# Kernel tuning notes

Measured on AMD Instinct MI355X. Metric: run time of the kernel, lower is better.

## Reference

```python
import jax, jax.numpy as jnp
import numpy as np

N, B, F = 204800, 4096, 256

def setup_inputs() -> dict:
    key = jax.random.key(0)
    ks = jax.random.split(key, 8)
    s = 1.0 / np.sqrt(F)
    return {
        'node_feats': jax.random.normal(ks[0], (N, F), jnp.float32),
        'g_feats': jax.random.normal(ks[1], (B, F), jnp.float32),
        'segment_ids': jnp.sort(jax.random.randint(ks[2], (N,), 0, B, jnp.int32)),
        'W_logit': jax.random.normal(ks[3], (1, 2 * F), jnp.float32) * (1.0 / np.sqrt(2 * F)),
        'b_logit': jnp.zeros((1,), jnp.float32),
        'W_proj': jax.random.normal(ks[4], (F, F), jnp.float32) * s,
        'b_proj': jnp.zeros((F,), jnp.float32),
        'W_ih': jax.random.normal(ks[5], (3 * F, F), jnp.float32) * s,
        'W_hh': jax.random.normal(ks[6], (3 * F, F), jnp.float32) * s,
        'b_ih': jnp.zeros((3 * F,), jnp.float32),
        'b_hh': jnp.zeros((3 * F,), jnp.float32),
    }

def reference(node_feats, g_feats, segment_ids, W_logit, b_logit, W_proj, b_proj, W_ih, W_hh, b_ih, b_hh):
    num_graphs = g_feats.shape[0]
    # logits: Linear(2F -> 1) on [broadcast(relu(g_feats)), node_feats], then LeakyReLU(0.01)
    ctx_nodes = jax.nn.relu(g_feats)[segment_ids]                      # [N, F]
    z = jnp.concatenate([ctx_nodes, node_feats], axis=1) @ W_logit.T + b_logit  # [N, 1]
    z = jax.nn.leaky_relu(z, negative_slope=0.01)
    # per-graph segment softmax over nodes
    zmax = jax.ops.segment_max(z, segment_ids, num_segments=num_graphs)
    z_exp = jnp.exp(z - zmax[segment_ids])
    denom = jax.ops.segment_sum(z_exp, segment_ids, num_segments=num_graphs)
    a = z_exp / denom[segment_ids]                                     # [N, 1]
    # project nodes (Dropout is identity at eval) and weighted segment sum
    hv = node_feats @ W_proj.T + b_proj                                # [N, F]
    g_repr = jax.ops.segment_sum(a * hv, segment_ids, num_segments=num_graphs)  # [B, F]
    context = jax.nn.elu(g_repr)
    # PyTorch GRUCell: input=context, hidden=g_feats
    gi = context @ W_ih.T + b_ih                                       # [B, 3F]
    gh = g_feats @ W_hh.T + b_hh
    i_r, i_z, i_n = jnp.split(gi, 3, axis=1)
    h_r, h_z, h_n = jnp.split(gh, 3, axis=1)
    r = jax.nn.sigmoid(i_r + h_r)
    zg = jax.nn.sigmoid(i_z + h_z)
    n = jnp.tanh(i_n + r * h_n)
    return (1.0 - zg) * n + zg * g_feats
```

## Files before the change

### kernel.cpp

```cpp
#include <hip/hip_runtime.h>

#define NN 204800
#define BB 4096
#define FF 256
#define CAP 72

typedef unsigned short u16;
typedef unsigned int u32;
typedef short bf16x8 __attribute__((ext_vector_type(8)));
typedef float f32x4  __attribute__((ext_vector_type(4)));

__device__ __forceinline__ u16 rne_bf16(float f){
    union { u32 v; float f; } t; t.f = f;
    u32 lsb = (t.v >> 16) & 1u;
    t.v += 0x7fffu + lsb;
    return (u16)(t.v >> 16);
}
__device__ __forceinline__ float bf16_to_f(u16 h){
    union { u32 v; float f; } t; t.v = (u32)h << 16; return t.f;
}
__device__ __forceinline__ void cvt4(const float* __restrict__ src, u16* __restrict__ dst){
    float4 v = *(const float4*)src;
    ushort4 h;
    h.x = rne_bf16(v.x); h.y = rne_bf16(v.y);
    h.z = rne_bf16(v.z); h.w = rne_bf16(v.w);
    *(ushort4*)dst = h;
}

__global__ void k_prep(const float* __restrict__ gfe, const float* __restrict__ Wp,
                       const float* __restrict__ Wih, const float* __restrict__ Whh,
                       const int* __restrict__ seg, int* __restrict__ start,
                       u16* __restrict__ gfe_b, u16* __restrict__ Wp_b,
                       u16* __restrict__ Wih_b, u16* __restrict__ Whh_b){
    int i = blockIdx.x * 256 + threadIdx.x;
    if (i <= BB){
        int lo = 0, hi = NN;
        while (lo < hi){ int mid = (lo + hi) >> 1; if (seg[mid] < i) lo = mid + 1; else hi = mid; }
        start[i] = lo;
    }
    const int n_gfe = BB * FF;
    const int n_wp  = FF * FF;
    const int n_w3  = 3 * FF * FF;
    int j = i * 4;
    if (j < n_gfe){ cvt4(gfe + j, gfe_b + j); return; }
    j -= n_gfe;
    if (j < n_wp){ cvt4(Wp + j, Wp_b + j); return; }
    j -= n_wp;
    if (j < n_w3){ cvt4(Wih + j, Wih_b + j); return; }
    j -= n_w3;
    if (j < n_w3){ cvt4(Whh + j, Whh_b + j); return; }
}
#define PREP_V4 ((BB*FF + FF*FF + 2*3*FF*FF) / 4)

__global__ __launch_bounds__(256) void k_attn(
        const float* __restrict__ x, const float* __restrict__ Wl,
        const float* __restrict__ bl, const float* __restrict__ gfe,
        const int* __restrict__ start, u16* __restrict__ s_b){
    __shared__ __align__(16) u16 xs[CAP][FF];
    __shared__ float zs[512];
    __shared__ float red[16];
    int g = blockIdx.x;
    int s0 = start[g], cnt = start[g + 1] - s0;
    int tid = threadIdx.x, wave = tid >> 6, lane = tid & 63;
    if (cnt == 0){
        s_b[(size_t)g * FF + tid] = 0;
        return;
    }
    float p = Wl[tid] * fmaxf(gfe[(size_t)g * FF + tid], 0.f);
    #pragma unroll
    for (int o = 32; o; o >>= 1) p += __shfl_xor(p, o);
    if (lane == 0) red[8 + wave] = p;
    float blv = bl[0];
    float4 wv = *(const float4*)(Wl + FF + lane * 4);

    auto st_row = [&](int row, const float4& v){
        ushort4 h;
        h.x = rne_bf16(v.x); h.y = rne_bf16(v.y);
        h.z = rne_bf16(v.z); h.w = rne_bf16(v.w);
        *(ushort4*)(&xs[row][lane * 4]) = h;
    };

    int i = wave;
    for (; i + 12 < cnt; i += 16){
        const float* r0 = x + (size_t)(s0 + i) * FF + lane * 4;
        float4 xv0 = *(const float4*)(r0);
        float4 xv1 = *(const float4*)(r0 + 4 * FF);
        float4 xv2 = *(const float4*)(r0 + 8 * FF);
        float4 xv3 = *(const float4*)(r0 + 12 * FF);
        float d0 = xv0.x * wv.x + xv0.y * wv.y + xv0.z * wv.z + xv0.w * wv.w;
        float d1 = xv1.x * wv.x + xv1.y * wv.y + xv1.z * wv.z + xv1.w * wv.w;
        float d2 = xv2.x * wv.x + xv2.y * wv.y + xv2.z * wv.z + xv2.w * wv.w;
        float d3 = xv3.x * wv.x + xv3.y * wv.y + xv3.z * wv.z + xv3.w * wv.w;
        #pragma unroll
        for (int o = 32; o; o >>= 1){
            d0 += __shfl_xor(d0, o); d1 += __shfl_xor(d1, o);
            d2 += __shfl_xor(d2, o); d3 += __shfl_xor(d3, o);
        }
        if (i      < CAP) st_row(i,      xv0);
        if (i + 4  < CAP) st_row(i + 4,  xv1);
        if (i + 8  < CAP) st_row(i + 8,  xv2);
        if (i + 12 < CAP) st_row(i + 12, xv3);
        if (lane == 0){
            zs[i] = d0; zs[i + 4] = d1; zs[i + 8] = d2; zs[i + 12] = d3;
        }
    }
    for (; i < cnt; i += 4){
        float4 xv = *(const float4*)(x + (size_t)(s0 + i) * FF + lane * 4);
        float d = xv.x * wv.x + xv.y * wv.y + xv.z * wv.z + xv.w * wv.w;
        #pragma unroll
        for (int o = 32; o; o >>= 1) d += __shfl_xor(d, o);
        if (i < CAP) st_row(i, xv);
        if (lane == 0) zs[i] = d;
    }
    __syncthreads();
    float cg = red[8] + red[9] + red[10] + red[11] + blv;
    float mx = -3.4e38f;
    for (int k = tid; k < cnt; k += 256){
        float t = cg + zs[k];
        t = t >= 0.f ? t : 0.01f * t;
        zs[k] = t;
        mx = fmaxf(mx, t);
    }
    #pragma unroll
    for (int o = 32; o; o >>= 1) mx = fmaxf(mx, __shfl_xor(mx, o));
    if (lane == 0) red[wave] = mx;
    __syncthreads();
    mx = fmaxf(fmaxf(red[0], red[1]), fmaxf(red[2], red[3]));
    float dsum = 0.f;
    for (int k = tid; k < cnt; k += 256){
        float e = expf(zs[k] - mx);
        zs[k] = e;
        dsum += e;
    }
    #pragma unroll
    for (int o = 32; o; o >>= 1) dsum += __shfl_xor(dsum, o);
    if (lane == 0) red[4 + wave] = dsum;
    __syncthreads();
    float inv = 1.f / (red[4] + red[5] + red[6] + red[7]);
    float acc = 0.f;
    int lim = cnt < CAP ? cnt : CAP;
    for (int k = 0; k < lim; k++) acc += zs[k] * bf16_to_f(xs[k][tid]);
    for (int k = CAP; k < cnt; k++) acc += zs[k] * x[(size_t)(s0 + k) * FF + tid];
    s_b[(size_t)g * FF + tid] = rne_bf16(acc * inv);
}

__global__ __launch_bounds__(256) void k_proj_mfma(
        const u16* __restrict__ s_b, const u16* __restrict__ Wp_b,
        const float* __restrict__ bp, const int* __restrict__ gate,
        u16* __restrict__ ctx_b){
    int tid = threadIdx.x;
    int w = tid >> 6, l = tid & 63;
    int mn = l & 15, q = l >> 4;
    int m0 = blockIdx.x * 64 + w * 16;
    int f0 = blockIdx.y * 64;
    f32x4 acc[4] = {};
    const u16* arow = s_b + (size_t)(m0 + mn) * FF + q * 8;
    #pragma unroll
    for (int kb = 0; kb < 8; kb++){
        bf16x8 a = *(const bf16x8*)(arow + kb * 32);
        #pragma unroll
        for (int cc = 0; cc < 4; cc++){
            bf16x8 b = *(const bf16x8*)(Wp_b + (size_t)(f0 + cc * 16 + mn) * FF + kb * 32 + q * 8);
            acc[cc] = __builtin_amdgcn_mfma_f32_16x16x32_bf16(a, b, acc[cc], 0, 0, 0);
        }
    }
    #pragma unroll
    for (int cc = 0; cc < 4; cc++){
        int f = f0 + cc * 16 + mn;
        float bias = bp[f];
        #pragma unroll
        for (int r = 0; r < 4; r++){
            int g = m0 + q * 4 + r;
            float bs = (gate[g + 1] > gate[g]) ? 1.f : 0.f;
            float v = acc[cc][r] + bs * bias;
            v = v > 0.f ? v : expm1f(v);
            ctx_b[(size_t)g * FF + f] = rne_bf16(v);
        }
    }
}

__global__ __launch_bounds__(256) void k_gru_mfma(
        const u16* __restrict__ ctx_b, const u16* __restrict__ gfe_b,
        const u16* __restrict__ Wih_b, const u16* __restrict__ Whh_b,
        const float* __restrict__ bih, const float* __restrict__ bhh,
        const float* __restrict__ gfe, float* __restrict__ out){
    int tid = threadIdx.x;
    int w = tid >> 6, l = tid & 63;
    int mn = l & 15, q = l >> 4;
    int g0 = blockIdx.x * 64 + w * 16;
    int f0 = blockIdx.y * 64;
    f32x4 ai[3][4] = {};
    f32x4 ah[3][4] = {};
    const u16* ac_row = ctx_b + (size_t)(g0 + mn) * FF + q * 8;
    const u16* ag_row = gfe_b + (size_t)(g0 + mn) * FF + q * 8;
    #pragma unroll
    for (int kb = 0; kb < 8; kb++){
        bf16x8 a_c = *(const bf16x8*)(ac_row + kb * 32);
        bf16x8 a_g = *(const bf16x8*)(ag_row + kb * 32);
        #pragma unroll
        for (int s = 0; s < 3; s++){
            #pragma unroll
            for (int cc = 0; cc < 4; cc++){
                size_t woff = (size_t)(s * FF + f0 + cc * 16 + mn) * FF + kb * 32 + q * 8;
                bf16x8 bi = *(const bf16x8*)(Wih_b + woff);
                ai[s][cc] = __builtin_amdgcn_mfma_f32_16x16x32_bf16(a_c, bi, ai[s][cc], 0, 0, 0);
                bf16x8 bh = *(const bf16x8*)(Whh_b + woff);
                ah[s][cc] = __builtin_amdgcn_mfma_f32_16x16x32_bf16(a_g, bh, ah[s][cc], 0, 0, 0);
            }
        }
    }
    #pragma unroll
    for (int cc = 0; cc < 4; cc++){
        int f = f0 + cc * 16 + mn;
        float bir = bih[f], biz = bih[FF + f], bin_ = bih[2 * FF + f];
        float bhr = bhh[f], bhz = bhh[FF + f], bhn = bhh[2 * FF + f];
        #pragma unroll
        for (int r = 0; r < 4; r++){
            int g = g0 + q * 4 + r;
            float rg = 1.f / (1.f + expf(-(ai[0][cc][r] + bir + ah[0][cc][r] + bhr)));
            float zg = 1.f / (1.f + expf(-(ai[1][cc][r] + biz + ah[1][cc][r] + bhz)));
            float ng = tanhf(ai[2][cc][r] + bin_ + rg * (ah[2][cc][r] + bhn));
            float h = gfe[(size_t)g * FF + f];
            out[(size_t)g * FF + f] = (1.f - zg) * ng + zg * h;
        }
    }
}

extern "C" void kernel_launch(void* const* d_in, const int* in_sizes, int n_in,
                              void* d_out, int out_size, void* d_ws, size_t ws_size,
                              hipStream_t stream){
    const float* node = (const float*)d_in[0];
    const float* gfe  = (const float*)d_in[1];
    const int*   seg  = (const int*)d_in[2];
    const float* Wl   = (const float*)d_in[3];
    const float* bl   = (const float*)d_in[4];
    const float* Wp   = (const float*)d_in[5];
    const float* bp   = (const float*)d_in[6];
    const float* Wih  = (const float*)d_in[7];
    const float* Whh  = (const float*)d_in[8];
    const float* bih  = (const float*)d_in[9];
    const float* bhh  = (const float*)d_in[10];
    float* out = (float*)d_out;

    char* p = (char*)d_ws;
    auto alloc = [&](size_t bytes)->void*{
        void* r = (void*)p; p += (bytes + 255) & ~(size_t)255; return r;
    };
    int*   start = (int*)  alloc((BB + 1) * sizeof(int));
    u16*   s_b   = (u16*)  alloc((size_t)BB * FF * sizeof(u16));
    u16*   ctx_b = (u16*)  alloc((size_t)BB * FF * sizeof(u16));
    u16*   gfe_b = (u16*)  alloc((size_t)BB * FF * sizeof(u16));
    u16*   Wp_b  = (u16*)  alloc((size_t)FF * FF * sizeof(u16));
    u16*   Wih_b = (u16*)  alloc((size_t)3 * FF * FF * sizeof(u16));
    u16*   Whh_b = (u16*)  alloc((size_t)3 * FF * FF * sizeof(u16));

    k_prep<<<(PREP_V4 + 255) / 256, 256, 0, stream>>>(gfe, Wp, Wih, Whh, seg, start,
                                                      gfe_b, Wp_b, Wih_b, Whh_b);
    k_attn<<<BB, 256, 0, stream>>>(node, Wl, bl, gfe, start, s_b);
    k_proj_mfma<<<dim3(BB / 64, FF / 64), 256, 0, stream>>>(s_b, Wp_b, bp, start, ctx_b);
    k_gru_mfma<<<dim3(BB / 64, FF / 64), 256, 0, stream>>>(ctx_b, gfe_b, Wih_b, Whh_b,
                                                           bih, bhh, gfe, out);
}
```

Before: 370.1 us.

## Fuse projection and GRU kernels via shared-memory context; nontemporal node loads

Merges the projection+ELU kernel and the GRU kernel into one launch. Each block of 512 threads computes a 16-graph context tile into LDS and then immediately runs the GRU GEMMs on it, so the bf16 context no longer round-trips through global memory and one launch is removed. Node-feature loads in the attention kernel are also switched to nontemporal loads so the streaming input does less cache pollution. The fused kernel uses smaller M tiles (16 rows), so every block re-reads the full weight matrices, which raises total weight traffic through L2.

```diff
diff --git a/kernel.cpp b/kernel.cpp
--- a/kernel.cpp
+++ b/kernel.cpp
@@ -9,6 +9,7 @@
 typedef unsigned int u32;
 typedef short bf16x8 __attribute__((ext_vector_type(8)));
 typedef float f32x4  __attribute__((ext_vector_type(4)));
+typedef float f4     __attribute__((ext_vector_type(4)));
 
 __device__ __forceinline__ u16 rne_bf16(float f){
     union { u32 v; float f; } t; t.f = f;
@@ -71,9 +72,9 @@
     for (int o = 32; o; o >>= 1) p += __shfl_xor(p, o);
     if (lane == 0) red[8 + wave] = p;
     float blv = bl[0];
-    float4 wv = *(const float4*)(Wl + FF + lane * 4);
-
-    auto st_row = [&](int row, const float4& v){
+    f4 wv = *(const f4*)(Wl + FF + lane * 4);
+
+    auto st_row = [&](int row, const f4& v){
         ushort4 h;
         h.x = rne_bf16(v.x); h.y = rne_bf16(v.y);
         h.z = rne_bf16(v.z); h.w = rne_bf16(v.w);
@@ -82,11 +83,11 @@
 
     int i = wave;
     for (; i + 12 < cnt; i += 16){
-        const float* r0 = x + (size_t)(s0 + i) * FF + lane * 4;
-        float4 xv0 = *(const float4*)(r0);
-        float4 xv1 = *(const float4*)(r0 + 4 * FF);
-        float4 xv2 = *(const float4*)(r0 + 8 * FF);
-        float4 xv3 = *(const float4*)(r0 + 12 * FF);
+        const f4* r0 = (const f4*)(x + (size_t)(s0 + i) * FF + lane * 4);
+        f4 xv0 = __builtin_nontemporal_load(r0);
+        f4 xv1 = __builtin_nontemporal_load(r0 + FF);
+        f4 xv2 = __builtin_nontemporal_load(r0 + 2 * FF);
+        f4 xv3 = __builtin_nontemporal_load(r0 + 3 * FF);
         float d0 = xv0.x * wv.x + xv0.y * wv.y + xv0.z * wv.z + xv0.w * wv.w;
         float d1 = xv1.x * wv.x + xv1.y * wv.y + xv1.z * wv.z + xv1.w * wv.w;
         float d2 = xv2.x * wv.x + xv2.y * wv.y + xv2.z * wv.z + xv2.w * wv.w;
@@ -105,7 +106,7 @@
         }
     }
     for (; i < cnt; i += 4){
-        float4 xv = *(const float4*)(x + (size_t)(s0 + i) * FF + lane * 4);
+        f4 xv = *(const f4*)(x + (size_t)(s0 + i) * FF + lane * 4);
         float d = xv.x * wv.x + xv.y * wv.y + xv.z * wv.z + xv.w * wv.w;
         #pragma unroll
         for (int o = 32; o; o >>= 1) d += __shfl_xor(d, o);
@@ -144,64 +145,57 @@
     s_b[(size_t)g * FF + tid] = rne_bf16(acc * inv);
 }
 
-__global__ __launch_bounds__(256) void k_proj_mfma(
+#define CPAD 264
+__global__ __launch_bounds__(512) void k_proj_gru(
         const u16* __restrict__ s_b, const u16* __restrict__ Wp_b,
-        const float* __restrict__ bp, const int* __restrict__ gate,
-        u16* __restrict__ ctx_b){
+        const float* __restrict__ bp, const int* __restrict__ start,
+        const u16* __restrict__ gfe_b, const u16* __restrict__ Wih_b,
+        const u16* __restrict__ Whh_b, const float* __restrict__ bih,
+        const float* __restrict__ bhh, const float* __restrict__ gfe,
+        float* __restrict__ out){
+    __shared__ __align__(16) u16 ctx_s[16][CPAD];
     int tid = threadIdx.x;
     int w = tid >> 6, l = tid & 63;
     int mn = l & 15, q = l >> 4;
-    int m0 = blockIdx.x * 64 + w * 16;
-    int f0 = blockIdx.y * 64;
-    f32x4 acc[4] = {};
-    const u16* arow = s_b + (size_t)(m0 + mn) * FF + q * 8;
+    int g0 = blockIdx.x * 16;
+    int fb = w * 32;
+    f32x4 acc[2] = {};
+    const u16* arow = s_b + (size_t)(g0 + mn) * FF + q * 8;
     #pragma unroll
     for (int kb = 0; kb < 8; kb++){
         bf16x8 a = *(const bf16x8*)(arow + kb * 32);
         #pragma unroll
-        for (int cc = 0; cc < 4; cc++){
-            bf16x8 b = *(const bf16x8*)(Wp_b + (size_t)(f0 + cc * 16 + mn) * FF + kb * 32 + q * 8);
+        for (int cc = 0; cc < 2; cc++){
+            bf16x8 b = *(const bf16x8*)(Wp_b + (size_t)(fb + cc * 16 + mn) * FF + kb * 32 + q * 8);
             acc[cc] = __builtin_amdgcn_mfma_f32_16x16x32_bf16(a, b, acc[cc], 0, 0, 0);
         }
     }
     #pragma unroll
-    for (int cc = 0; cc < 4; cc++){
-        int f = f0 + cc * 16 + mn;
+    for (int cc = 0; cc < 2; cc++){
+        int f = fb + cc * 16 + mn;
         float bias = bp[f];
         #pragma unroll
         for (int r = 0; r < 4; r++){
-            int g = m0 + q * 4 + r;
-            float bs = (gate[g + 1] > gate[g]) ? 1.f : 0.f;
+            int g = g0 + q * 4 + r;
+            float bs = (start[g + 1] > start[g]) ? 1.f : 0.f;
             float v = acc[cc][r] + bs * bias;
             v = v > 0.f ? v : expm1f(v);
-            ctx_b[(size_t)g * FF + f] = rne_bf16(v);
-        }
-    }
-}
-
-__global__ __launch_bounds__(256) void k_gru_mfma(
-        const u16* __restrict__ ctx_b, const u16* __restrict__ gfe_b,
-        const u16* __restrict__ Wih_b, const u16* __restrict__ Whh_b,
-        const float* __restrict__ bih, const float* __restrict__ bhh,
-        const float* __restrict__ gfe, float* __restrict__ out){
-    int tid = threadIdx.x;
-    int w = tid >> 6, l = tid & 63;
-    int mn = l & 15, q = l >> 4;
-    int g0 = blockIdx.x * 64 + w * 16;
-    int f0 = blockIdx.y * 64;
-    f32x4 ai[3][4] = {};
-    f32x4 ah[3][4] = {};
-    const u16* ac_row = ctx_b + (size_t)(g0 + mn) * FF + q * 8;
+            ctx_s[q * 4 + r][f] = rne_bf16(v);
+        }
+    }
+    __syncthreads();
+    f32x4 ai[3][2] = {};
+    f32x4 ah[3][2] = {};
     const u16* ag_row = gfe_b + (size_t)(g0 + mn) * FF + q * 8;
     #pragma unroll
     for (int kb = 0; kb < 8; kb++){
-        bf16x8 a_c = *(const bf16x8*)(ac_row + kb * 32);
+        bf16x8 a_c = *(const bf16x8*)(&ctx_s[mn][kb * 32 + q * 8]);
         bf16x8 a_g = *(const bf16x8*)(ag_row + kb * 32);
         #pragma unroll
         for (int s = 0; s < 3; s++){
             #pragma unroll
-            for (int cc = 0; cc < 4; cc++){
-                size_t woff = (size_t)(s * FF + f0 + cc * 16 + mn) * FF + kb * 32 + q * 8;
+            for (int cc = 0; cc < 2; cc++){
+                size_t woff = (size_t)(s * FF + fb + cc * 16 + mn) * FF + kb * 32 + q * 8;
                 bf16x8 bi = *(const bf16x8*)(Wih_b + woff);
                 ai[s][cc] = __builtin_amdgcn_mfma_f32_16x16x32_bf16(a_c, bi, ai[s][cc], 0, 0, 0);
                 bf16x8 bh = *(const bf16x8*)(Whh_b + woff);
@@ -210,8 +204,8 @@
         }
     }
     #pragma unroll
-    for (int cc = 0; cc < 4; cc++){
-        int f = f0 + cc * 16 + mn;
+    for (int cc = 0; cc < 2; cc++){
+        int f = fb + cc * 16 + mn;
         float bir = bih[f], biz = bih[FF + f], bin_ = bih[2 * FF + f];
         float bhr = bhh[f], bhz = bhh[FF + f], bhn = bhh[2 * FF + f];
         #pragma unroll
@@ -248,7 +242,6 @@
     };
     int*   start = (int*)  alloc((BB + 1) * sizeof(int));
     u16*   s_b   = (u16*)  alloc((size_t)BB * FF * sizeof(u16));
-    u16*   ctx_b = (u16*)  alloc((size_t)BB * FF * sizeof(u16));
     u16*   gfe_b = (u16*)  alloc((size_t)BB * FF * sizeof(u16));
     u16*   Wp_b  = (u16*)  alloc((size_t)FF * FF * sizeof(u16));
     u16*   Wih_b = (u16*)  alloc((size_t)3 * FF * FF * sizeof(u16));
@@ -257,7 +250,6 @@
     k_prep<<<(PREP_V4 + 255) / 256, 256, 0, stream>>>(gfe, Wp, Wih, Whh, seg, start,
                                                       gfe_b, Wp_b, Wih_b, Whh_b);
     k_attn<<<BB, 256, 0, stream>>>(node, Wl, bl, gfe, start, s_b);
-    k_proj_mfma<<<dim3(BB / 64, FF / 64), 256, 0, stream>>>(s_b, Wp_b, bp, start, ctx_b);
-    k_gru_mfma<<<dim3(BB / 64, FF / 64), 256, 0, stream>>>(ctx_b, gfe_b, Wih_b, Whh_b,
-                                                           bih, bhh, gfe, out);
-}
+    k_proj_gru<<<BB / 16, 512, 0, stream>>>(s_b, Wp_b, bp, start, gfe_b, Wih_b, Whh_b,
+                                            bih, bhh, gfe, out);
+}
```

Result: faster. 343.8 us (-7.1%).
